# Optimization experiments

Measured on AMD Instinct MI355X. Metric: run time of the kernel, lower is better.

## Reference

```python
import jax, jax.numpy as jnp
import numpy as np

B, L, D, DI, DS, DC, DTR = 128, 31, 1024, 2048, 16, 5, 64

def setup_inputs() -> dict:
    key = jax.random.key(0)
    ks = jax.random.split(key, 12)
    rn = lambda k, shp, s=0.02: jax.random.normal(k, shp, dtype=jnp.float32) * s
    return {
        "x": jax.random.normal(ks[0], (B, L, D), dtype=jnp.float32),
        "norm1_w": jnp.ones((D,), jnp.float32), "norm1_b": jnp.zeros((D,), jnp.float32),
        "in_proj_W": rn(ks[1], (2 * DI, D)),
        "conv_w": rn(ks[2], (DI, DC), 0.2), "conv_b": jnp.zeros((DI,), jnp.float32),
        "x_proj_W": rn(ks[3], (DTR + 2 * DS, DI)),
        "dt_proj_W": rn(ks[4], (DI, DTR), 0.1),
        "dt_proj_b": jnp.full((DI,), -4.6, dtype=jnp.float32),  # softplus^-1(~0.01)
        "A_log": jnp.tile(jnp.log(jnp.arange(1, DS + 1, dtype=jnp.float32))[None, :], (DI, 1)),
        "D_ssm": jnp.ones((DI,), jnp.float32),
        "out_proj_W": rn(ks[5], (D, DI)),
        "norm2_w": jnp.ones((D,), jnp.float32), "norm2_b": jnp.zeros((D,), jnp.float32),
        "ffn_W1": rn(ks[6], (2 * D, D)), "ffn_b1": jnp.zeros((2 * D,), jnp.float32),
        "ffn_W2": rn(ks[7], (D, 2 * D)), "ffn_b2": jnp.zeros((D,), jnp.float32),
        "cls_W1": rn(ks[8], (D, L * D)), "cls_b1": jnp.zeros((D,), jnp.float32),
        "cls_W2": rn(ks[9], (1, D)), "cls_b2": jnp.zeros((1,), jnp.float32),
    }

def _ln(x, w, b):
    m = x.mean(-1, keepdims=True)
    v = x.var(-1, keepdims=True)
    return (x - m) * jax.lax.rsqrt(v + 1e-5) * w + b

def _mamba(x, in_proj_W, conv_w, conv_b, x_proj_W, dt_proj_W, dt_proj_b, A_log, D_ssm, out_proj_W):
    # in_proj -> (u, z)
    xz = jnp.einsum('bld,ed->ble', x, in_proj_W)            # (B,L,2*DI)
    u, z = jnp.split(xz, 2, axis=-1)
    # causal depthwise conv1d (kernel DC) + SiLU
    xp = jnp.pad(u, ((0, 0), (DC - 1, 0), (0, 0)))
    uc = conv_b + sum(xp[:, k:k + L, :] * conv_w[:, k] for k in range(DC))
    uc = jax.nn.silu(uc)
    # input-dependent dt, B, C
    x_dbl = jnp.einsum('bld,ed->ble', uc, x_proj_W)         # (B,L,DTR+2*DS)
    dt, Bm, Cm = jnp.split(x_dbl, [DTR, DTR + DS], axis=-1)
    dt = jax.nn.softplus(jnp.einsum('blr,dr->bld', dt, dt_proj_W) + dt_proj_b)
    A = -jnp.exp(A_log)                                      # (DI,DS)
    def step(h, ins):
        dt_t, B_t, C_t, u_t = ins                            # (B,DI),(B,DS),(B,DS),(B,DI)
        dA = jnp.exp(dt_t[:, :, None] * A)                   # (B,DI,DS)
        h = h * dA + dt_t[:, :, None] * B_t[:, None, :] * u_t[:, :, None]
        y = jnp.einsum('bds,bs->bd', h, C_t)
        return h, y
    h0 = jnp.zeros((u.shape[0], DI, DS), u.dtype)
    _, ys = jax.lax.scan(step, h0, (dt.transpose(1, 0, 2), Bm.transpose(1, 0, 2),
                                    Cm.transpose(1, 0, 2), uc.transpose(1, 0, 2)))
    y = ys.transpose(1, 0, 2) + uc * D_ssm                   # skip term D*u
    y = y * jax.nn.silu(z)                                   # gate
    return jnp.einsum('bld,ed->ble', y, out_proj_W)

def reference(x, norm1_w, norm1_b, in_proj_W, conv_w, conv_b, x_proj_W, dt_proj_W,
              dt_proj_b, A_log, D_ssm, out_proj_W, norm2_w, norm2_b, ffn_W1, ffn_b1,
              ffn_W2, ffn_b2, cls_W1, cls_b1, cls_W2, cls_b2):
    # single encoder block (n_layers=1), dropout = identity (eval)
    res = x
    h = _ln(x, norm1_w, norm1_b)
    h = _mamba(h, in_proj_W, conv_w, conv_b, x_proj_W, dt_proj_W, dt_proj_b,
               A_log, D_ssm, out_proj_W)
    x = res + h
    res = x
    h = _ln(x, norm2_w, norm2_b)
    h = jax.nn.silu(jnp.einsum('bld,ed->ble', h, ffn_W1) + ffn_b1)
    h = jnp.einsum('ble,de->bld', h, ffn_W2) + ffn_b2
    x = res + h
    # classifier: Flatten -> Linear -> SiLU -> Linear
    flat = x.reshape(x.shape[0], -1)                          # (B, L*D)
    c = jax.nn.silu(flat @ cls_W1.T + cls_b1)
    out = c @ cls_W2.T + cls_b2                               # (B,1)
    return (out, x)
```

## Files before the change

kernel.cpp:

```cpp
#include <hip/hip_runtime.h>
#include <cstddef>
#include <cstdint>

#define B_   128
#define L_   31
#define D_   1024
#define DI_  2048
#define DS_  16
#define DC_  5
#define DTR_ 64
#define ROWS (B_ * L_)
#define KCLS (L_ * D_)

#define W_IN  0
#define W_OUT 4194304
#define W_F1  6291456
#define W_F2  8388608
#define W_XP  10485760
#define W_DT  10747904
#define WTOT  10878976

typedef unsigned short u16;
typedef __attribute__((ext_vector_type(8))) short s16x8;
typedef __attribute__((ext_vector_type(4))) float f32x4;

__device__ __forceinline__ float silu_f(float x) { return x / (1.0f + __expf(-x)); }

__device__ __forceinline__ u16 f2b(float f) {
    union { float f; uint32_t u; } c; c.f = f;
    uint32_t u = c.u + 0x7FFF + ((c.u >> 16) & 1);
    return (u16)(u >> 16);
}
__device__ __forceinline__ float b2f(u16 b) {
    union { uint32_t u; float f; } c; c.u = ((uint32_t)b) << 16;
    return c.f;
}
__device__ __forceinline__ uint32_t pack2(float lo, float hi) {
    return (uint32_t)f2b(lo) | ((uint32_t)f2b(hi) << 16);
}
__device__ __forceinline__ void cvt8(const float* __restrict__ s, u16* __restrict__ d) {
    const float4* p = (const float4*)s;
    float4 a = p[0], b = p[1];
    uint4 r;
    r.x = pack2(a.x, a.y); r.y = pack2(a.z, a.w);
    r.z = pack2(b.x, b.y); r.w = pack2(b.z, b.w);
    *(uint4*)d = r;
}

#define GLD16(g, s) __builtin_amdgcn_global_load_lds( \
    (const __attribute__((address_space(1))) void*)(g), \
    (__attribute__((address_space(3))) void*)(s), 16, 0, 0)

__global__ __launch_bounds__(256) void f2b_all_kernel(
    const float* __restrict__ inW, const float* __restrict__ outW,
    const float* __restrict__ f1W, const float* __restrict__ f2W,
    const float* __restrict__ xpW, const float* __restrict__ dtW,
    u16* __restrict__ wbuf)
{
    int g = blockIdx.x * 256 + threadIdx.x;
    if (g < 524288) { cvt8(inW + (size_t)g * 8, wbuf + W_IN + (size_t)g * 8); return; }
    g -= 524288;
    if (g < 262144) { cvt8(outW + (size_t)g * 8, wbuf + W_OUT + (size_t)g * 8); return; }
    g -= 262144;
    if (g < 262144) { cvt8(f1W + (size_t)g * 8, wbuf + W_F1 + (size_t)g * 8); return; }
    g -= 262144;
    if (g < 262144) { cvt8(f2W + (size_t)g * 8, wbuf + W_F2 + (size_t)g * 8); return; }
    g -= 262144;
    if (g < 32768) {
        const int row = g >> 8, col8 = (g & 255) * 8;
        u16* d = wbuf + W_XP + (size_t)row * 2048 + col8;
        if (row < 96) cvt8(xpW + (size_t)row * 2048 + col8, d);
        else *(uint4*)d = make_uint4(0, 0, 0, 0);
        return;
    }
    g -= 32768;
    if (g < 16384) cvt8(dtW + (size_t)g * 8, wbuf + W_DT + (size_t)g * 8);
}

__global__ __launch_bounds__(256) void ln_kernel(const float* __restrict__ x,
                                                 const float* __restrict__ w,
                                                 const float* __restrict__ b,
                                                 u16* __restrict__ y)
{
    const int row = blockIdx.x;
    const float* xr = x + (size_t)row * D_;
    float v[4];
    float sum = 0.f, sq = 0.f;
#pragma unroll
    for (int i = 0; i < 4; i++) {
        v[i] = xr[threadIdx.x + i * 256];
        sum += v[i];
        sq  += v[i] * v[i];
    }
#pragma unroll
    for (int o = 32; o > 0; o >>= 1) {
        sum += __shfl_down(sum, o, 64);
        sq  += __shfl_down(sq, o, 64);
    }
    __shared__ float red[8];
    const int wid = threadIdx.x >> 6;
    if ((threadIdx.x & 63) == 0) { red[wid] = sum; red[4 + wid] = sq; }
    __syncthreads();
    sum = red[0] + red[1] + red[2] + red[3];
    sq  = red[4] + red[5] + red[6] + red[7];
    const float mean = sum * (1.0f / D_);
    const float var  = sq * (1.0f / D_) - mean * mean;
    const float rstd = rsqrtf(var + 1e-5f);
    u16* yr = y + (size_t)row * D_;
#pragma unroll
    for (int i = 0; i < 4; i++) {
        const int c = threadIdx.x + i * 256;
        yr[c] = f2b((v[i] - mean) * rstd * w[c] + b[c]);
    }
}

__global__ __launch_bounds__(256) void ln2_fuse_kernel(const float* __restrict__ x,
                                                       const float* __restrict__ p0,
                                                       const float* __restrict__ p1,
                                                       const float* __restrict__ w,
                                                       const float* __restrict__ b,
                                                       float* __restrict__ x2,
                                                       u16* __restrict__ y)
{
    const int row = blockIdx.x;
    const size_t base = (size_t)row * D_;
    float v[4];
    float sum = 0.f, sq = 0.f;
#pragma unroll
    for (int i = 0; i < 4; i++) {
        const int c = threadIdx.x + i * 256;
        const float s = x[base + c] + p0[base + c] + p1[base + c];
        x2[base + c] = s;
        v[i] = s;
        sum += s;
        sq  += s * s;
    }
#pragma unroll
    for (int o = 32; o > 0; o >>= 1) {
        sum += __shfl_down(sum, o, 64);
        sq  += __shfl_down(sq, o, 64);
    }
    __shared__ float red[8];
    const int wid = threadIdx.x >> 6;
    if ((threadIdx.x & 63) == 0) { red[wid] = sum; red[4 + wid] = sq; }
    __syncthreads();
    sum = red[0] + red[1] + red[2] + red[3];
    sq  = red[4] + red[5] + red[6] + red[7];
    const float mean = sum * (1.0f / D_);
    const float var  = sq * (1.0f / D_) - mean * mean;
    const float rstd = rsqrtf(var + 1e-5f);
    u16* yr = y + base;
#pragma unroll
    for (int i = 0; i < 4; i++) {
        const int c = threadIdx.x + i * 256;
        yr[c] = f2b((v[i] - mean) * rstd * w[c] + b[c]);
    }
}

__global__ __launch_bounds__(256) void add3_bias_kernel(const float* __restrict__ x2,
                                                        const float* __restrict__ q0,
                                                        const float* __restrict__ q1,
                                                        const float* __restrict__ b2,
                                                        float* __restrict__ x3)
{
    const int i = blockIdx.x * 256 + threadIdx.x;
    float4 a  = ((const float4*)x2)[i];
    float4 c0 = ((const float4*)q0)[i];
    float4 c1 = ((const float4*)q1)[i];
    float4 bb = ((const float4*)b2)[i & 255];
    float4 r;
    r.x = a.x + c0.x + c1.x + bb.x;
    r.y = a.y + c0.y + c1.y + bb.y;
    r.z = a.z + c0.z + c1.z + bb.z;
    r.w = a.w + c0.w + c1.w + bb.w;
    ((float4*)x3)[i] = r;
}

template <int ACT, bool BIAS, int OUT>
__global__ __launch_bounds__(256) void gemm128_bk64(
    const u16* __restrict__ A, const u16* __restrict__ W,
    const float* __restrict__ bias, void* __restrict__ Cout,
    int M, int K, int Nout, int kLen)
{
    __shared__ __align__(16) u16 As[128 * 64];
    __shared__ __align__(16) u16 Bs[128 * 64];
    const int tid = threadIdx.x;
    const int l = tid & 63, w = tid >> 6;
    const int bm = blockIdx.y * 128, bn = blockIdx.x * 128;
    const int kOff = blockIdx.z * kLen;

    const int srow = tid >> 3;
    const int sg   = tid & 7;
    const int sgx  = sg ^ (srow & 7);
    const u16* gA = A + (size_t)(bm + srow) * K + kOff + sgx * 8;
    const u16* gB = W + (size_t)(bn + srow) * K + kOff + sgx * 8;
    const int soff = srow * 64 + sg * 8;

    const int lane15 = l & 15, lhi = l >> 4;
    const int key = lane15 & 7;
    const int wr = w >> 1, wc = w & 1;
    const u16* fArow = As + (wr * 64 + lane15) * 64;
    const u16* fBrow = Bs + (wc * 64 + lane15) * 64;

    f32x4 acc[4][4] = {};

    for (int kk = 0; kk < kLen; kk += 64) {
#pragma unroll
        for (int c = 0; c < 4; c++) {
            GLD16(gA + (size_t)c * 32 * K, As + c * 2048 + soff);
            GLD16(gB + (size_t)c * 32 * K, Bs + c * 2048 + soff);
        }
        gA += 64; gB += 64;
        __syncthreads();
#pragma unroll
        for (int ks = 0; ks < 2; ks++) {
            const int gsel = ((ks * 4 + lhi) ^ key) * 8;
            s16x8 af[4], bfr[4];
#pragma unroll
            for (int mi = 0; mi < 4; mi++) af[mi]  = *(const s16x8*)(fArow + mi * 16 * 64 + gsel);
#pragma unroll
            for (int ni = 0; ni < 4; ni++) bfr[ni] = *(const s16x8*)(fBrow + ni * 16 * 64 + gsel);
#pragma unroll
            for (int mi = 0; mi < 4; mi++)
#pragma unroll
                for (int ni = 0; ni < 4; ni++)
                    acc[mi][ni] = __builtin_amdgcn_mfma_f32_16x16x32_bf16(
                        af[mi], bfr[ni], acc[mi][ni], 0, 0, 0);
        }
        __syncthreads();
    }

#pragma unroll
    for (int ni = 0; ni < 4; ni++) {
        const int col = bn + wc * 64 + ni * 16 + lane15;
        const float bv = BIAS ? bias[col] : 0.0f;
#pragma unroll
        for (int mi = 0; mi < 4; mi++) {
#pragma unroll
            for (int r = 0; r < 4; r++) {
                const int row = bm + wr * 64 + mi * 16 + lhi * 4 + r;
                float v = acc[mi][ni][r] + bv;
                if (ACT == 1) v = silu_f(v);
                if (OUT == 1) ((u16*)Cout)[(size_t)row * Nout + col] = f2b(v);
                else          ((float*)Cout)[((size_t)blockIdx.z * M + row) * Nout + col] = v;
            }
        }
    }
}

template <int ACT, bool BIAS, int OUT>
__global__ __launch_bounds__(256) void gemm_mfma(
    const u16* __restrict__ A, const u16* __restrict__ W,
    const float* __restrict__ bias, void* __restrict__ Cout,
    int M, int K, int Nout, int kLen)
{
    __shared__ __align__(16) u16 As[128 * 32];
    __shared__ __align__(16) u16 Bs[128 * 32];
    const int tid = threadIdx.x;
    const int l = tid & 63, w = tid >> 6;
    const int bm = blockIdx.y * 128, bn = blockIdx.x * 128;
    const int kOff = blockIdx.z * kLen;

    const int sr = l >> 2;
    const int sk = (l & 3) * 8;
    const u16* gA = A + (size_t)(bm + w * 16 + sr) * K + kOff + sk;
    const u16* gB = W + (size_t)(bn + w * 16 + sr) * K + kOff + sk;
    u16* lA = As + (w * 16 + sr) * 32 + sk;
    u16* lB = Bs + (w * 16 + sr) * 32 + sk;

    const int lane15 = l & 15, lhi = l >> 4;
    const int wr = w >> 1, wc = w & 1;
    const u16* fA = As + (wr * 64 + lane15) * 32 + lhi * 8;
    const u16* fB = Bs + (wc * 64 + lane15) * 32 + lhi * 8;

    f32x4 acc[4][4] = {};

    for (int kk = 0; kk < kLen; kk += 32) {
        GLD16(gA, lA); GLD16(gA + (size_t)64 * K, lA + 64 * 32);
        GLD16(gB, lB); GLD16(gB + (size_t)64 * K, lB + 64 * 32);
        gA += 32; gB += 32;
        __syncthreads();
        s16x8 af[4], bfr[4];
#pragma unroll
        for (int mi = 0; mi < 4; mi++) af[mi]  = *(const s16x8*)(fA + mi * 16 * 32);
#pragma unroll
        for (int ni = 0; ni < 4; ni++) bfr[ni] = *(const s16x8*)(fB + ni * 16 * 32);
#pragma unroll
        for (int mi = 0; mi < 4; mi++)
#pragma unroll
            for (int ni = 0; ni < 4; ni++)
                acc[mi][ni] = __builtin_amdgcn_mfma_f32_16x16x32_bf16(
                    af[mi], bfr[ni], acc[mi][ni], 0, 0, 0);
        __syncthreads();
    }

#pragma unroll
    for (int ni = 0; ni < 4; ni++) {
        const int col = bn + wc * 64 + ni * 16 + lane15;
        if (col >= Nout) continue;
        const float bv = BIAS ? bias[col] : 0.0f;
#pragma unroll
        for (int mi = 0; mi < 4; mi++) {
#pragma unroll
            for (int r = 0; r < 4; r++) {
                const int row = bm + wr * 64 + mi * 16 + lhi * 4 + r;
                float v = acc[mi][ni][r] + bv;
                if (ACT == 2) v = (v > 20.0f) ? v : log1pf(__expf(v));
                if (OUT == 1) ((u16*)Cout)[(size_t)row * Nout + col] = f2b(v);
                if (OUT == 2) atomicAdd(&((float*)Cout)[(size_t)row * Nout + col], v);
            }
        }
    }
}

#define KCH 512
__global__ __launch_bounds__(256) void gemm_cls_mfma(
    const float* __restrict__ A, const float* __restrict__ W,
    float* __restrict__ C)
{
    __shared__ __align__(16) u16 As[128 * 32];
    __shared__ __align__(16) u16 Bs[128 * 32];
    const int tid = threadIdx.x;
    const int l = tid & 63, w = tid >> 6;
    const int bn = blockIdx.x * 128;
    const int k0 = blockIdx.y * KCH;

    const int sr = l >> 2;
    const int sk = (l & 3) * 8;
    const int row = w * 16 + sr;
    const float* gA0 = A + (size_t)row * KCLS + k0 + sk;
    const float* gA1 = gA0 + (size_t)64 * KCLS;
    const float* gB0 = W + (size_t)(bn + row) * KCLS + k0 + sk;
    const float* gB1 = gB0 + (size_t)64 * KCLS;
    u16* lA0 = As + row * 32 + sk;  u16* lA1 = lA0 + 64 * 32;
    u16* lB0 = Bs + row * 32 + sk;  u16* lB1 = lB0 + 64 * 32;

    const int lane15 = l & 15, lhi = l >> 4;
    const int wr = w >> 1, wc = w & 1;
    const u16* fA = As + (wr * 64 + lane15) * 32 + lhi * 8;
    const u16* fB = Bs + (wc * 64 + lane15) * 32 + lhi * 8;

    f32x4 acc[4][4] = {};

    for (int ks = 0; ks < KCH / 32; ks++) {
        float4 a00 = *(const float4*)(gA0);     float4 a01 = *(const float4*)(gA0 + 4);
        float4 a10 = *(const float4*)(gA1);     float4 a11 = *(const float4*)(gA1 + 4);
        float4 b00 = *(const float4*)(gB0);     float4 b01 = *(const float4*)(gB0 + 4);
        float4 b10 = *(const float4*)(gB1);     float4 b11 = *(const float4*)(gB1 + 4);
        gA0 += 32; gA1 += 32; gB0 += 32; gB1 += 32;
        __syncthreads();
        uint4 r;
        r.x = pack2(a00.x, a00.y); r.y = pack2(a00.z, a00.w);
        r.z = pack2(a01.x, a01.y); r.w = pack2(a01.z, a01.w);
        *(uint4*)lA0 = r;
        r.x = pack2(a10.x, a10.y); r.y = pack2(a10.z, a10.w);
        r.z = pack2(a11.x, a11.y); r.w = pack2(a11.z, a11.w);
        *(uint4*)lA1 = r;
        r.x = pack2(b00.x, b00.y); r.y = pack2(b00.z, b00.w);
        r.z = pack2(b01.x, b01.y); r.w = pack2(b01.z, b01.w);
        *(uint4*)lB0 = r;
        r.x = pack2(b10.x, b10.y); r.y = pack2(b10.z, b10.w);
        r.z = pack2(b11.x, b11.y); r.w = pack2(b11.z, b11.w);
        *(uint4*)lB1 = r;
        __syncthreads();
        s16x8 af[4], bfr[4];
#pragma unroll
        for (int mi = 0; mi < 4; mi++) af[mi]  = *(const s16x8*)(fA + mi * 16 * 32);
#pragma unroll
        for (int ni = 0; ni < 4; ni++) bfr[ni] = *(const s16x8*)(fB + ni * 16 * 32);
#pragma unroll
        for (int mi = 0; mi < 4; mi++)
#pragma unroll
            for (int ni = 0; ni < 4; ni++)
                acc[mi][ni] = __builtin_amdgcn_mfma_f32_16x16x32_bf16(
                    af[mi], bfr[ni], acc[mi][ni], 0, 0, 0);
    }

#pragma unroll
    for (int ni = 0; ni < 4; ni++) {
        const int col = bn + wc * 64 + ni * 16 + lane15;
#pragma unroll
        for (int mi = 0; mi < 4; mi++) {
#pragma unroll
            for (int r = 0; r < 4; r++) {
                const int m = wr * 64 + mi * 16 + lhi * 4 + r;
                atomicAdd(&C[(size_t)m * 1024 + col], acc[mi][ni][r]);
            }
        }
    }
}

__global__ __launch_bounds__(256) void conv_silu_kernel(const u16* __restrict__ xz,
                                                        const float* __restrict__ cw,
                                                        const float* __restrict__ cb,
                                                        u16* __restrict__ uc)
{
    const int idx = blockIdx.x * 256 + threadIdx.x;
    const int d  = idx & (DI_ - 1);
    const int bl = idx >> 11;
    const int l  = bl % L_;
    const int b  = bl / L_;
    const u16* u = xz + (size_t)b * L_ * (2 * DI_) + d;
    float acc = cb[d];
#pragma unroll
    for (int k = 0; k < DC_; k++) {
        const int ll = l + k - (DC_ - 1);
        if (ll >= 0) acc = fmaf(b2f(u[(size_t)ll * (2 * DI_)]), cw[d * DC_ + k], acc);
    }
    uc[(size_t)bl * DI_ + d] = f2b(silu_f(acc));
}

__global__ __launch_bounds__(256) void dtext_kernel(const float* __restrict__ xdbl,
                                                    u16* __restrict__ dtb)
{
    const int idx = blockIdx.x * 256 + threadIdx.x;
    const int row = idx >> 4, c4 = (idx & 15) * 4;
    float4 v = *(const float4*)(xdbl + (size_t)row * 96 + c4);
    uint2 r;
    r.x = pack2(v.x, v.y); r.y = pack2(v.z, v.w);
    *(uint2*)(dtb + (size_t)row * 64 + c4) = r;
}

__global__ __launch_bounds__(256) void scan_kernel(const u16* __restrict__ dt,
                                                   const u16* __restrict__ uc,
                                                   const u16* __restrict__ xz,
                                                   const float* __restrict__ xdbl,
                                                   const float* __restrict__ A_log,
                                                   const float* __restrict__ D_ssm,
                                                   u16* __restrict__ y)
{
    const int idx = blockIdx.x * 256 + threadIdx.x;
    const int d = idx & (DI_ - 1);
    const int b = idx >> 11;
    float A[DS_];
#pragma unroll
    for (int s = 0; s < DS_; s++) A[s] = -__expf(A_log[d * DS_ + s]);
    const float Dv = D_ssm[d];
    float h[DS_] = {};
    for (int l = 0; l < L_; l++) {
        const size_t bl = (size_t)b * L_ + l;
        const float dtv = b2f(dt[bl * DI_ + d]);
        const float uv  = b2f(uc[bl * DI_ + d]);
        const float zv  = b2f(xz[bl * (2 * DI_) + DI_ + d]);
        const float* Bp = xdbl + bl * (DTR_ + 2 * DS_) + DTR_;
        const float* Cp = Bp + DS_;
        float yv = 0.f;
#pragma unroll
        for (int s = 0; s < DS_; s++) {
            h[s] = fmaf(h[s], __expf(dtv * A[s]), dtv * Bp[s] * uv);
            yv = fmaf(h[s], Cp[s], yv);
        }
        yv = fmaf(uv, Dv, yv);
        yv *= silu_f(zv);
        y[bl * DI_ + d] = f2b(yv);
    }
}

__global__ __launch_bounds__(256) void cls2_kernel(const float* __restrict__ c,
                                                   const float* __restrict__ b1,
                                                   const float* __restrict__ W2,
                                                   const float* __restrict__ b2,
                                                   float* __restrict__ out)
{
    const int b = blockIdx.x;
    float s = 0.f;
    for (int n = threadIdx.x; n < D_; n += 256) {
        float v = c[b * D_ + n] + b1[n];
        v = silu_f(v);
        s = fmaf(v, W2[n], s);
    }
#pragma unroll
    for (int o = 32; o > 0; o >>= 1) s += __shfl_down(s, o, 64);
    __shared__ float red[4];
    const int wid = threadIdx.x >> 6;
    if ((threadIdx.x & 63) == 0) red[wid] = s;
    __syncthreads();
    if (threadIdx.x == 0) out[b] = red[0] + red[1] + red[2] + red[3] + b2[0];
}

extern "C" void kernel_launch(void* const* d_in, const int* in_sizes, int n_in,
                              void* d_out, int out_size, void* d_ws, size_t ws_size,
                              hipStream_t stream)
{
    const float* x         = (const float*)d_in[0];
    const float* n1w       = (const float*)d_in[1];
    const float* n1b       = (const float*)d_in[2];
    const float* in_projW  = (const float*)d_in[3];
    const float* conv_w    = (const float*)d_in[4];
    const float* conv_b    = (const float*)d_in[5];
    const float* x_projW   = (const float*)d_in[6];
    const float* dt_projW  = (const float*)d_in[7];
    const float* dt_projb  = (const float*)d_in[8];
    const float* A_log     = (const float*)d_in[9];
    const float* D_ssm     = (const float*)d_in[10];
    const float* out_projW = (const float*)d_in[11];
    const float* n2w       = (const float*)d_in[12];
    const float* n2b       = (const float*)d_in[13];
    const float* ffn_W1    = (const float*)d_in[14];
    const float* ffn_b1    = (const float*)d_in[15];
    const float* ffn_W2    = (const float*)d_in[16];
    const float* ffn_b2    = (const float*)d_in[17];
    const float* cls_W1    = (const float*)d_in[18];
    const float* cls_b1    = (const float*)d_in[19];
    const float* cls_W2    = (const float*)d_in[20];
    const float* cls_b2    = (const float*)d_in[21];

    u16* base   = (u16*)d_ws;
    u16* xz_b   = base;
    u16* uc_b   = xz_b + (size_t)ROWS * 4096;
    u16* dt_b   = uc_b + (size_t)ROWS * 2048;
    u16* y_b    = dt_b + (size_t)ROWS * 2048;
    u16* h_b    = y_b + (size_t)ROWS * 2048;
    float* x2   = (float*)(h_b + (size_t)ROWS * 1024);
    float* xdbl = x2 + (size_t)ROWS * 1024;
    u16* dtb    = (u16*)(xdbl + (size_t)ROWS * 96);
    u16* wbuf   = dtb + (size_t)ROWS * 64;
    float* clsh = (float*)(wbuf + (size_t)WTOT);
    float* pq   = clsh + (size_t)B_ * D_;

    float* outv = (float*)d_out;
    float* x3   = outv + B_;

    f2b_all_kernel<<<dim3(5312), dim3(256), 0, stream>>>(
        in_projW, out_projW, ffn_W1, ffn_W2, x_projW, dt_projW, wbuf);
    ln_kernel<<<dim3(ROWS), dim3(256), 0, stream>>>(x, n1w, n1b, h_b);
    gemm128_bk64<0, false, 1><<<dim3(32, 31, 1), dim3(256), 0, stream>>>(
        h_b, wbuf + W_IN, nullptr, xz_b, ROWS, D_, 2 * DI_, D_);
    conv_silu_kernel<<<dim3(ROWS * DI_ / 256), dim3(256), 0, stream>>>(xz_b, conv_w, conv_b, uc_b);
    hipMemsetAsync(xdbl, 0, (size_t)ROWS * 96 * sizeof(float), stream);
    gemm_mfma<0, false, 2><<<dim3(1, 31, 16), dim3(256), 0, stream>>>(
        uc_b, wbuf + W_XP, nullptr, xdbl, ROWS, DI_, DTR_ + 2 * DS_, 128);
    dtext_kernel<<<dim3(ROWS * 16 / 256), dim3(256), 0, stream>>>(xdbl, dtb);
    gemm_mfma<2, true, 1><<<dim3(16, 31, 1), dim3(256), 0, stream>>>(
        dtb, wbuf + W_DT, dt_projb, dt_b, ROWS, DTR_, DI_, DTR_);
    scan_kernel<<<dim3(B_ * DI_ / 256), dim3(256), 0, stream>>>(
        dt_b, uc_b, xz_b, xdbl, A_log, D_ssm, y_b);
    gemm128_bk64<0, false, 3><<<dim3(8, 31, 2), dim3(256), 0, stream>>>(
        y_b, wbuf + W_OUT, nullptr, pq, ROWS, DI_, D_, 1024);
    ln2_fuse_kernel<<<dim3(ROWS), dim3(256), 0, stream>>>(
        x, pq, pq + (size_t)ROWS * D_, n2w, n2b, x2, h_b);
    gemm128_bk64<1, true, 1><<<dim3(16, 31, 1), dim3(256), 0, stream>>>(
        h_b, wbuf + W_F1, ffn_b1, uc_b, ROWS, D_, 2 * D_, D_);
    gemm128_bk64<0, false, 3><<<dim3(8, 31, 2), dim3(256), 0, stream>>>(
        uc_b, wbuf + W_F2, nullptr, pq, ROWS, 2 * D_, D_, 1024);
    add3_bias_kernel<<<dim3(ROWS * D_ / 4 / 256), dim3(256), 0, stream>>>(
        x2, pq, pq + (size_t)ROWS * D_, ffn_b2, x3);
    hipMemsetAsync(clsh, 0, (size_t)B_ * D_ * sizeof(float), stream);
    gemm_cls_mfma<<<dim3(1024 / 128, KCLS / KCH), dim3(256), 0, stream>>>(x3, cls_W1, clsh);
    cls2_kernel<<<dim3(B_), dim3(256), 0, stream>>>(clsh, cls_b1, cls_W2, cls_b2, outv);
}
```

Baseline: 392.1 us.

## Prefetch cls GEMM tiles, swizzle LDS, vectorize conv, unify small GEMMs

The classifier GEMM now keeps its next global fp32 tile in registers while the current tile is converted and multiplied. It also XOR-swizzles its LDS layout to cut bank conflicts and replaces the syncthreads with raw barriers. The depthwise conv kernel now handles 8 channels per thread with 16-byte loads and stores. The separate gemm_mfma kernel is removed and the x_proj and dt_proj GEMMs are routed through gemm128_bk64, which gains bounds checks and the extra epilogue modes. The BK=64 tile assumes K is a multiple of 64, which holds for K=64 and kLen=128. Prefetching raises register pressure.

```diff
diff --git a/kernel.cpp b/kernel.cpp
--- a/kernel.cpp
+++ b/kernel.cpp
@@ -233,6 +233,7 @@
 #pragma unroll
     for (int ni = 0; ni < 4; ni++) {
         const int col = bn + wc * 64 + ni * 16 + lane15;
+        if (col >= Nout) continue;
         const float bv = BIAS ? bias[col] : 0.0f;
 #pragma unroll
         for (int mi = 0; mi < 4; mi++) {
@@ -241,73 +242,10 @@
                 const int row = bm + wr * 64 + mi * 16 + lhi * 4 + r;
                 float v = acc[mi][ni][r] + bv;
                 if (ACT == 1) v = silu_f(v);
-                if (OUT == 1) ((u16*)Cout)[(size_t)row * Nout + col] = f2b(v);
-                else          ((float*)Cout)[((size_t)blockIdx.z * M + row) * Nout + col] = v;
-            }
-        }
-    }
-}
-
-template <int ACT, bool BIAS, int OUT>
-__global__ __launch_bounds__(256) void gemm_mfma(
-    const u16* __restrict__ A, const u16* __restrict__ W,
-    const float* __restrict__ bias, void* __restrict__ Cout,
-    int M, int K, int Nout, int kLen)
-{
-    __shared__ __align__(16) u16 As[128 * 32];
-    __shared__ __align__(16) u16 Bs[128 * 32];
-    const int tid = threadIdx.x;
-    const int l = tid & 63, w = tid >> 6;
-    const int bm = blockIdx.y * 128, bn = blockIdx.x * 128;
-    const int kOff = blockIdx.z * kLen;
-
-    const int sr = l >> 2;
-    const int sk = (l & 3) * 8;
-    const u16* gA = A + (size_t)(bm + w * 16 + sr) * K + kOff + sk;
-    const u16* gB = W + (size_t)(bn + w * 16 + sr) * K + kOff + sk;
-    u16* lA = As + (w * 16 + sr) * 32 + sk;
-    u16* lB = Bs + (w * 16 + sr) * 32 + sk;
-
-    const int lane15 = l & 15, lhi = l >> 4;
-    const int wr = w >> 1, wc = w & 1;
-    const u16* fA = As + (wr * 64 + lane15) * 32 + lhi * 8;
-    const u16* fB = Bs + (wc * 64 + lane15) * 32 + lhi * 8;
-
-    f32x4 acc[4][4] = {};
-
-    for (int kk = 0; kk < kLen; kk += 32) {
-        GLD16(gA, lA); GLD16(gA + (size_t)64 * K, lA + 64 * 32);
-        GLD16(gB, lB); GLD16(gB + (size_t)64 * K, lB + 64 * 32);
-        gA += 32; gB += 32;
-        __syncthreads();
-        s16x8 af[4], bfr[4];
-#pragma unroll
-        for (int mi = 0; mi < 4; mi++) af[mi]  = *(const s16x8*)(fA + mi * 16 * 32);
-#pragma unroll
-        for (int ni = 0; ni < 4; ni++) bfr[ni] = *(const s16x8*)(fB + ni * 16 * 32);
-#pragma unroll
-        for (int mi = 0; mi < 4; mi++)
-#pragma unroll
-            for (int ni = 0; ni < 4; ni++)
-                acc[mi][ni] = __builtin_amdgcn_mfma_f32_16x16x32_bf16(
-                    af[mi], bfr[ni], acc[mi][ni], 0, 0, 0);
-        __syncthreads();
-    }
-
-#pragma unroll
-    for (int ni = 0; ni < 4; ni++) {
-        const int col = bn + wc * 64 + ni * 16 + lane15;
-        if (col >= Nout) continue;
-        const float bv = BIAS ? bias[col] : 0.0f;
-#pragma unroll
-        for (int mi = 0; mi < 4; mi++) {
-#pragma unroll
-            for (int r = 0; r < 4; r++) {
-                const int row = bm + wr * 64 + mi * 16 + lhi * 4 + r;
-                float v = acc[mi][ni][r] + bv;
                 if (ACT == 2) v = (v > 20.0f) ? v : log1pf(__expf(v));
                 if (OUT == 1) ((u16*)Cout)[(size_t)row * Nout + col] = f2b(v);
                 if (OUT == 2) atomicAdd(&((float*)Cout)[(size_t)row * Nout + col], v);
+                if (OUT == 3) ((float*)Cout)[((size_t)blockIdx.z * M + row) * Nout + col] = v;
             }
         }
     }
@@ -325,30 +263,36 @@
     const int bn = blockIdx.x * 128;
     const int k0 = blockIdx.y * KCH;
 
-    const int sr = l >> 2;
-    const int sk = (l & 3) * 8;
+    const int sr  = l >> 2;
+    const int sgl = l & 3;
     const int row = w * 16 + sr;
-    const float* gA0 = A + (size_t)row * KCLS + k0 + sk;
+    const int skw = ((sgl ^ (sr & 3))) * 8;
+    const float* gA0 = A + (size_t)row * KCLS + k0 + sgl * 8;
     const float* gA1 = gA0 + (size_t)64 * KCLS;
-    const float* gB0 = W + (size_t)(bn + row) * KCLS + k0 + sk;
+    const float* gB0 = W + (size_t)(bn + row) * KCLS + k0 + sgl * 8;
     const float* gB1 = gB0 + (size_t)64 * KCLS;
-    u16* lA0 = As + row * 32 + sk;  u16* lA1 = lA0 + 64 * 32;
-    u16* lB0 = Bs + row * 32 + sk;  u16* lB1 = lB0 + 64 * 32;
+    u16* lA0 = As + row * 32 + skw;  u16* lA1 = lA0 + 64 * 32;
+    u16* lB0 = Bs + row * 32 + skw;  u16* lB1 = lB0 + 64 * 32;
 
     const int lane15 = l & 15, lhi = l >> 4;
     const int wr = w >> 1, wc = w & 1;
-    const u16* fA = As + (wr * 64 + lane15) * 32 + lhi * 8;
-    const u16* fB = Bs + (wc * 64 + lane15) * 32 + lhi * 8;
+    const int rsel = (lhi ^ (lane15 & 3)) * 8;
+    const u16* fA = As + (wr * 64 + lane15) * 32 + rsel;
+    const u16* fB = Bs + (wc * 64 + lane15) * 32 + rsel;
 
     f32x4 acc[4][4] = {};
 
+    float4 a00 = *(const float4*)(gA0);  float4 a01 = *(const float4*)(gA0 + 4);
+    float4 a10 = *(const float4*)(gA1);  float4 a11 = *(const float4*)(gA1 + 4);
+    float4 b00 = *(const float4*)(gB0);  float4 b01 = *(const float4*)(gB0 + 4);
+    float4 b10 = *(const float4*)(gB1);  float4 b11 = *(const float4*)(gB1 + 4);
+
     for (int ks = 0; ks < KCH / 32; ks++) {
-        float4 a00 = *(const float4*)(gA0);     float4 a01 = *(const float4*)(gA0 + 4);
-        float4 a10 = *(const float4*)(gA1);     float4 a11 = *(const float4*)(gA1 + 4);
-        float4 b00 = *(const float4*)(gB0);     float4 b01 = *(const float4*)(gB0 + 4);
-        float4 b10 = *(const float4*)(gB1);     float4 b11 = *(const float4*)(gB1 + 4);
-        gA0 += 32; gA1 += 32; gB0 += 32; gB1 += 32;
-        __syncthreads();
+        if (ks) {
+            asm volatile("" ::: "memory");
+            __builtin_amdgcn_s_barrier();
+            asm volatile("" ::: "memory");
+        }
         uint4 r;
         r.x = pack2(a00.x, a00.y); r.y = pack2(a00.z, a00.w);
         r.z = pack2(a01.x, a01.y); r.w = pack2(a01.z, a01.w);
@@ -362,7 +306,16 @@
         r.x = pack2(b10.x, b10.y); r.y = pack2(b10.z, b10.w);
         r.z = pack2(b11.x, b11.y); r.w = pack2(b11.z, b11.w);
         *(uint4*)lB1 = r;
-        __syncthreads();
+        if (ks + 1 < KCH / 32) {
+            gA0 += 32; gA1 += 32; gB0 += 32; gB1 += 32;
+            a00 = *(const float4*)(gA0);  a01 = *(const float4*)(gA0 + 4);
+            a10 = *(const float4*)(gA1);  a11 = *(const float4*)(gA1 + 4);
+            b00 = *(const float4*)(gB0);  b01 = *(const float4*)(gB0 + 4);
+            b10 = *(const float4*)(gB1);  b11 = *(const float4*)(gB1 + 4);
+        }
+        asm volatile("s_waitcnt lgkmcnt(0)" ::: "memory");
+        __builtin_amdgcn_s_barrier();
+        asm volatile("" ::: "memory");
         s16x8 af[4], bfr[4];
 #pragma unroll
         for (int mi = 0; mi < 4; mi++) af[mi]  = *(const s16x8*)(fA + mi * 16 * 32);
@@ -396,18 +349,36 @@
                                                         u16* __restrict__ uc)
 {
     const int idx = blockIdx.x * 256 + threadIdx.x;
-    const int d  = idx & (DI_ - 1);
-    const int bl = idx >> 11;
+    const int d8 = idx & 255;
+    const int bl = idx >> 8;
     const int l  = bl % L_;
     const int b  = bl / L_;
-    const u16* u = xz + (size_t)b * L_ * (2 * DI_) + d;
-    float acc = cb[d];
+    const u16* ubase = xz + (size_t)b * L_ * (2 * DI_) + d8 * 8;
+
+    float acc[8];
+    const float4 cb0 = ((const float4*)cb)[d8 * 2];
+    const float4 cb1 = ((const float4*)cb)[d8 * 2 + 1];
+    acc[0] = cb0.x; acc[1] = cb0.y; acc[2] = cb0.z; acc[3] = cb0.w;
+    acc[4] = cb1.x; acc[5] = cb1.y; acc[6] = cb1.z; acc[7] = cb1.w;
+
 #pragma unroll
     for (int k = 0; k < DC_; k++) {
         const int ll = l + k - (DC_ - 1);
-        if (ll >= 0) acc = fmaf(b2f(u[(size_t)ll * (2 * DI_)]), cw[d * DC_ + k], acc);
-    }
-    uc[(size_t)bl * DI_ + d] = f2b(silu_f(acc));
+        if (ll < 0) continue;
+        const uint4 uv = *(const uint4*)(ubase + (size_t)ll * (2 * DI_));
+        const uint32_t uw[4] = {uv.x, uv.y, uv.z, uv.w};
+#pragma unroll
+        for (int j = 0; j < 8; j++) {
+            const float x = b2f((u16)(uw[j >> 1] >> ((j & 1) * 16)));
+            acc[j] = fmaf(x, cw[(d8 * 8 + j) * DC_ + k], acc[j]);
+        }
+    }
+    uint4 r;
+    r.x = pack2(silu_f(acc[0]), silu_f(acc[1]));
+    r.y = pack2(silu_f(acc[2]), silu_f(acc[3]));
+    r.z = pack2(silu_f(acc[4]), silu_f(acc[5]));
+    r.w = pack2(silu_f(acc[6]), silu_f(acc[7]));
+    *(uint4*)(uc + (size_t)bl * DI_ + d8 * 8) = r;
 }
 
 __global__ __launch_bounds__(256) void dtext_kernel(const float* __restrict__ xdbl,
@@ -526,12 +497,12 @@
     ln_kernel<<<dim3(ROWS), dim3(256), 0, stream>>>(x, n1w, n1b, h_b);
     gemm128_bk64<0, false, 1><<<dim3(32, 31, 1), dim3(256), 0, stream>>>(
         h_b, wbuf + W_IN, nullptr, xz_b, ROWS, D_, 2 * DI_, D_);
-    conv_silu_kernel<<<dim3(ROWS * DI_ / 256), dim3(256), 0, stream>>>(xz_b, conv_w, conv_b, uc_b);
+    conv_silu_kernel<<<dim3(ROWS), dim3(256), 0, stream>>>(xz_b, conv_w, conv_b, uc_b);
     hipMemsetAsync(xdbl, 0, (size_t)ROWS * 96 * sizeof(float), stream);
-    gemm_mfma<0, false, 2><<<dim3(1, 31, 16), dim3(256), 0, stream>>>(
+    gemm128_bk64<0, false, 2><<<dim3(1, 31, 16), dim3(256), 0, stream>>>(
         uc_b, wbuf + W_XP, nullptr, xdbl, ROWS, DI_, DTR_ + 2 * DS_, 128);
     dtext_kernel<<<dim3(ROWS * 16 / 256), dim3(256), 0, stream>>>(xdbl, dtb);
-    gemm_mfma<2, true, 1><<<dim3(16, 31, 1), dim3(256), 0, stream>>>(
+    gemm128_bk64<2, true, 1><<<dim3(16, 31, 1), dim3(256), 0, stream>>>(
         dtb, wbuf + W_DT, dt_projb, dt_b, ROWS, DTR_, DI_, DTR_);
     scan_kernel<<<dim3(B_ * DI_ / 256), dim3(256), 0, stream>>>(
         dt_b, uc_b, xz_b, xdbl, A_log, D_ssm, y_b);
```

Measured after the change: 437.1 us. 11.5% more time.
